# Performance work log

Hardware: AMD Instinct MI355X
Metric: run time of the kernel (lower is better)

The kernel has to match this reference:

```python
import jax, jax.numpy as jnp
import numpy as np

N_NODES = 50000
N_EDGES = 800000
IN_DIM = 128
OUT_DIM = 64
K_KERNELS = 2
S_ATTEN = 2


def setup_inputs() -> dict:
    key = jax.random.key(0)
    ks = jax.random.split(key, 9)
    return {
        "x": jax.random.normal(ks[0], (N_NODES, IN_DIM), dtype=jnp.float32),
        "support_vals": jax.random.uniform(ks[1], (K_KERNELS, N_EDGES), dtype=jnp.float32),
        "atten_vals": jax.random.uniform(ks[2], (S_ATTEN, N_EDGES), dtype=jnp.float32),
        "W_transform": jax.random.normal(ks[3], (K_KERNELS, IN_DIM, OUT_DIM), dtype=jnp.float32) * 0.05,
        "w_left": jax.random.normal(ks[4], (K_KERNELS, S_ATTEN + 1, OUT_DIM), dtype=jnp.float32) * 0.05,
        "w_right": jax.random.normal(ks[5], (K_KERNELS, S_ATTEN + 1, OUT_DIM), dtype=jnp.float32) * 0.05,
        "W_residual": jax.random.normal(ks[6], (IN_DIM + OUT_DIM, OUT_DIM), dtype=jnp.float32) * 0.05,
        "edge_rows": jax.random.randint(ks[7], (N_EDGES,), 0, N_NODES, dtype=jnp.int64),
        "edge_cols": jax.random.randint(ks[8], (N_EDGES,), 0, N_NODES, dtype=jnp.int64),
    }


def reference(x, support_vals, atten_vals, W_transform, w_left, w_right, W_residual, edge_rows, edge_cols):
    # x: [N, F], edge lists: [E]; all supports share the same sparsity pattern.
    N = x.shape[0]
    K = W_transform.shape[0]
    output = jnp.zeros((N, W_transform.shape[2]), dtype=x.dtype)
    for k in range(K):
        wx = x @ W_transform[k]                       # [N, D]
        al = wx @ w_left[k].T                         # [N, S+1]
        ar = wx @ w_right[k].T                        # [N, S+1]
        # per-support edge values; support i=S uses this kernel's Cheb support
        vals = jnp.concatenate([atten_vals, support_vals[k][None, :]], axis=0)  # [S+1, E]
        # score_e = sum_i (al[row_e,i] + ar[col_e,i]) * vals[i,e]
        scores = jnp.einsum('es,se->e', al[edge_rows] + ar[edge_cols], vals)    # [E]
        # row-wise (segment) softmax over nonzeros, as tf.sparse_softmax
        m = jax.ops.segment_max(scores, edge_rows, num_segments=N)              # [N]
        ex = jnp.exp(scores - m[edge_rows])
        denom = jax.ops.segment_sum(ex, edge_rows, num_segments=N)              # [N]
        probs = ex / denom[edge_rows]                                           # [E]
        # spmm: out[r] = sum_{e: row_e=r} probs_e * wx[col_e]
        output = output + jax.ops.segment_sum(probs[:, None] * wx[edge_cols], edge_rows, num_segments=N)
    # residual projection then elu activation
    output = jnp.concatenate([x, output], axis=-1) @ W_residual
    return jax.nn.elu(output)
```

## Files before the change

kernel.cpp:

```cpp
#include <hip/hip_runtime.h>

#define N_NODES 50000
#define N_EDGES 800000
#define IN_DIM 128
#define OUT_DIM 64
#define NEG_INF (-1e30f)
#define GBLK ((N_NODES + 63) / 64)
#define BSHIFT 7
#define NBUK ((N_NODES + 127) >> 7)
#define NBUKP 392
#define EB 1024
#define PREB ((N_EDGES + EB - 1) / EB)
#define NFRAG (3 * 16 + 8)
#define STAGE_CAP 3072

typedef unsigned short ushort_t;
typedef __attribute__((ext_vector_type(8))) short short8;
typedef __attribute__((ext_vector_type(4))) float f32x4;
typedef __attribute__((ext_vector_type(2))) _Float16 half2_t;

__device__ __forceinline__ unsigned f2bf(float f) {
    unsigned u = __float_as_uint(f);
    u += 0x7fffu + ((u >> 16) & 1u);
    return u >> 16;
}
__device__ __forceinline__ unsigned rl_u(unsigned v, int i) {
    return __builtin_amdgcn_readlane(v, i);
}
__device__ __forceinline__ unsigned pack_h2(float a, float b) {
    auto h = __builtin_amdgcn_cvt_pkrtz(a, b);
    union { decltype(h) h2; unsigned u; } v; v.h2 = h; return v.u;
}
__device__ __forceinline__ float dot2u(unsigned w, unsigned p, float acc) {
    union { unsigned u; half2_t h; } wv, pv;
    wv.u = w; pv.u = p;
    return __builtin_amdgcn_fdot2(wv.h, pv.h, acc, false);
}

__global__ void wpack_kernel(const float* __restrict__ Wt,
                             const float* __restrict__ Wres,
                             ushort_t* __restrict__ Wpack) {
    int idx = blockIdx.x * 256 + threadIdx.x;
    if (idx >= NFRAG * 512) return;
    int f = idx >> 9;
    int within = idx & 511;
    int lane = within >> 3;
    int b = within & 7;
    float val;
    if (f < 48) {
        int mat = f >> 4;
        int ct = (f >> 2) & 3;
        int kc = f & 3;
        int k = kc * 32 + (lane >> 4) * 8 + b;
        int c = ct * 16 + (lane & 15);
        const float* W = (mat < 2) ? (Wt + (size_t)mat * IN_DIM * OUT_DIM) : Wres;
        val = W[(size_t)k * OUT_DIM + c];
    } else {
        int f2 = f - 48;
        int ct = f2 >> 1;
        int kc = f2 & 1;
        int k = kc * 32 + (lane >> 4) * 8 + b;
        int c = ct * 16 + (lane & 15);
        val = Wres[(size_t)(IN_DIM + k) * OUT_DIM + c];
    }
    Wpack[idx] = (ushort_t)f2bf(val);
}

__global__ __launch_bounds__(256) void gemm_kernel(
        const float* __restrict__ x,
        const ushort_t* __restrict__ Wpack,
        const float* __restrict__ wl,
        const float* __restrict__ wr,
        unsigned* __restrict__ wxi,
        float* __restrict__ xres,
        float* __restrict__ al,
        float* __restrict__ ar) {
    int wave = threadIdx.x >> 6;
    int lane = threadIdx.x & 63;
    int lr = lane & 15;
    int lg = lane >> 4;
    int row0 = blockIdx.x * 64 + wave * 16;

    int arow = row0 + lr;
    if (arow >= N_NODES) arow = N_NODES - 1;
    const float* xr = x + (size_t)arow * IN_DIM;
    short8 afrag[4];
#pragma unroll
    for (int kc = 0; kc < 4; ++kc) {
        float4 f0 = *(const float4*)(xr + kc * 32 + lg * 8);
        float4 f1 = *(const float4*)(xr + kc * 32 + lg * 8 + 4);
        short8 a;
        a[0] = (short)f2bf(f0.x); a[1] = (short)f2bf(f0.y);
        a[2] = (short)f2bf(f0.z); a[3] = (short)f2bf(f0.w);
        a[4] = (short)f2bf(f1.x); a[5] = (short)f2bf(f1.y);
        a[6] = (short)f2bf(f1.z); a[7] = (short)f2bf(f1.w);
        afrag[kc] = a;
    }

    f32x4 acc[3][4] = {};
#pragma unroll
    for (int kc = 0; kc < 4; ++kc) {
#pragma unroll
        for (int mat = 0; mat < 3; ++mat) {
#pragma unroll
            for (int ct = 0; ct < 4; ++ct) {
                short8 bfrag = *(const short8*)(
                    Wpack + (size_t)(((mat * 4 + ct) * 4 + kc) << 9) + lane * 8);
                acc[mat][ct] = __builtin_amdgcn_mfma_f32_16x16x32_bf16(
                    afrag[kc], bfrag, acc[mat][ct], 0, 0, 0);
            }
        }
    }

#pragma unroll
    for (int r = 0; r < 4; ++r) {
        int gr = row0 + lg * 4 + r;
        if (gr < N_NODES) {
#pragma unroll
            for (int ct = 0; ct < 4; ++ct) {
                wxi[(size_t)gr * OUT_DIM + ct * 16 + lr] =
                    pack_h2(acc[0][ct][r], acc[1][ct][r]);
                xres[(size_t)gr * OUT_DIM + ct * 16 + lr] = acc[2][ct][r];
            }
        }
    }

#pragma unroll
    for (int mat = 0; mat < 2; ++mat) {
#pragma unroll
        for (int s = 0; s < 3; ++s) {
            float wlv[4], wrv[4];
#pragma unroll
            for (int ct = 0; ct < 4; ++ct) {
                wlv[ct] = wl[(size_t)(mat * 3 + s) * OUT_DIM + ct * 16 + lr];
                wrv[ct] = wr[(size_t)(mat * 3 + s) * OUT_DIM + ct * 16 + lr];
            }
#pragma unroll
            for (int r = 0; r < 4; ++r) {
                float pl = 0.f, pr = 0.f;
#pragma unroll
                for (int ct = 0; ct < 4; ++ct) {
                    pl = fmaf(acc[mat][ct][r], wlv[ct], pl);
                    pr = fmaf(acc[mat][ct][r], wrv[ct], pr);
                }
#pragma unroll
                for (int off = 1; off < 16; off <<= 1) {
                    pl += __shfl_xor(pl, off);
                    pr += __shfl_xor(pr, off);
                }
                if (lr == 0) {
                    int gr = row0 + lg * 4 + r;
                    if (gr < N_NODES) {
                        al[(size_t)gr * 6 + mat * 3 + s] = pl;
                        ar[(size_t)gr * 6 + mat * 3 + s] = pr;
                    }
                }
            }
        }
    }
}

__global__ __launch_bounds__(256) void score_sort_kernel(
        const int* __restrict__ rows,
        const int* __restrict__ cols,
        const float* __restrict__ atten,
        const float* __restrict__ support,
        const float* __restrict__ al,
        const float* __restrict__ ar,
        uint4* __restrict__ etmp,
        uint2* __restrict__ cl) {
    __shared__ int cnt[512];
    __shared__ int cur[512];
    __shared__ int aux[256];
    __shared__ uint4 stage[EB];
    int t = threadIdx.x;
    cnt[t] = 0; cnt[t + 256] = 0;
    __syncthreads();
    int base0 = blockIdx.x * EB;
    int nval = min(EB, N_EDGES - base0);

    int r_[4], c_[4];
    float s0_[4], s1_[4];
#pragma unroll
    for (int i = 0; i < 4; ++i) {
        int e = base0 + i * 256 + t;
        bool v = e < N_EDGES;
        int r = v ? rows[e] : -1;
        int c = v ? cols[e] : 0;
        float sc0 = 0.f, sc1 = 0.f;
        if (v) {
            float a0 = atten[e], a1 = atten[N_EDGES + e];
            float sp0 = support[e], sp1 = support[N_EDGES + e];
            const float* A = al + (size_t)r * 6;
            const float* B = ar + (size_t)c * 6;
            sc0 = (A[0] + B[0]) * a0 + (A[1] + B[1]) * a1 + (A[2] + B[2]) * sp0;
            sc1 = (A[3] + B[3]) * a0 + (A[4] + B[4]) * a1 + (A[5] + B[5]) * sp1;
            atomicAdd(&cnt[r >> BSHIFT], 1);
        }
        r_[i] = r; c_[i] = c; s0_[i] = sc0; s1_[i] = sc1;
    }
    __syncthreads();
    int a0 = cnt[2 * t], a1 = cnt[2 * t + 1];
    int ps = a0 + a1;
    aux[t] = ps;
    __syncthreads();
    int val = ps;
    for (int off = 1; off < 256; off <<= 1) {
        int y = (t >= off) ? aux[t - off] : 0;
        __syncthreads();
        val += y; aux[t] = val;
        __syncthreads();
    }
    int e2 = val - ps;
    cur[2 * t] = e2;
    cur[2 * t + 1] = e2 + a0;
    size_t cb = (size_t)blockIdx.x * NBUKP;
    if (2 * t < NBUK)     cl[cb + 2 * t]     = make_uint2((unsigned)a0, (unsigned)e2);
    if (2 * t + 1 < NBUK) cl[cb + 2 * t + 1] = make_uint2((unsigned)a1, (unsigned)(e2 + a0));
    __syncthreads();
#pragma unroll
    for (int i = 0; i < 4; ++i) {
        if (r_[i] < 0) continue;
        int pos = atomicAdd(&cur[r_[i] >> BSHIFT], 1);
        uint4 pv;
        pv.x = (unsigned)c_[i] | ((unsigned)(r_[i] & 127) << 16);
        pv.y = __float_as_uint(s0_[i]);
        pv.z = __float_as_uint(s1_[i]);
        pv.w = 0u;
        stage[pos] = pv;
    }
    __syncthreads();
    for (int i = t; i < nval; i += 256)
        etmp[(size_t)base0 + i] = stage[i];
}

__global__ void colscan_kernel(const uint2* __restrict__ cl,
                               int* __restrict__ btot) {
    __shared__ int sh[256];
    int k = blockIdx.x, t = threadIdx.x;
    int s = 0;
    for (int b = t; b < PREB; b += 256) s += (int)cl[(size_t)b * NBUKP + k].x;
    sh[t] = s;
    __syncthreads();
    for (int off = 128; off > 0; off >>= 1) {
        if (t < off) sh[t] += sh[t + off];
        __syncthreads();
    }
    if (t == 0) btot[k] = sh[0];
}

__global__ __launch_bounds__(256) void sortb_kernel(
        const uint2* __restrict__ cl,
        const int* __restrict__ btot,
        const uint4* __restrict__ etmp,
        uint4* __restrict__ edata,
        int* __restrict__ row_ptr) {
    __shared__ uint4 stage[STAGE_CAP];
    __shared__ int rpos[PREB + 2];
    __shared__ int lloff[PREB];
    __shared__ int aux[256];
    __shared__ int bb[512];
    __shared__ int hist[128], rcur[128];
    int k = blockIdx.x, t = threadIdx.x;

    bb[t] = (t < NBUK) ? btot[t] : 0;
    bb[t + 256] = (t + 256 < NBUK) ? btot[t + 256] : 0;
    __syncthreads();
    int a0 = bb[2 * t], a1 = bb[2 * t + 1];
    int ps = a0 + a1;
    aux[t] = ps;
    __syncthreads();
    int val = ps;
    for (int off = 1; off < 256; off <<= 1) {
        int y = (t >= off) ? aux[t - off] : 0;
        __syncthreads();
        val += y; aux[t] = val;
        __syncthreads();
    }
    bb[2 * t] = val - ps;
    bb[2 * t + 1] = val - ps + a0;
    __syncthreads();
    int base = bb[k];

    for (int b = t; b < PREB; b += 256) {
        uint2 v2 = cl[(size_t)b * NBUKP + k];
        rpos[b] = (int)v2.x;
        lloff[b] = (int)v2.y;
    }
    if (t < 128) hist[t] = 0;
    __syncthreads();
    int v[4];
    int idx4 = 4 * t;
#pragma unroll
    for (int i = 0; i < 4; ++i) v[i] = (idx4 + i < PREB) ? rpos[idx4 + i] : 0;
    __syncthreads();
    int s = 0;
#pragma unroll
    for (int i = 0; i < 4; ++i) { int tmp = v[i]; v[i] = s; s += tmp; }
    aux[t] = s;
    __syncthreads();
    int tv = s;
    for (int off = 1; off < 256; off <<= 1) {
        int y = (t >= off) ? aux[t - off] : 0;
        __syncthreads();
        tv += y; aux[t] = tv;
        __syncthreads();
    }
    int ofs = tv - s;
#pragma unroll
    for (int i = 0; i < 4; ++i)
        if (idx4 + i <= PREB) rpos[idx4 + i] = ofs + v[i];
    __syncthreads();
    int nb = rpos[PREB];

    for (int b = t; b < PREB; b += 256) {
        int s0 = rpos[b];
        int n = rpos[b + 1] - s0;
        int lo = lloff[b];
        const uint4* src = etmp + (size_t)b * EB + lo;
        for (int i = 0; i < n; ++i) {
            uint4 rec = src[i];
            int j = s0 + i;
            if (j < STAGE_CAP) stage[j] = rec;
            atomicAdd(&hist[(rec.x >> 16) & 127], 1);
        }
    }
    __syncthreads();
    int hv = (t < 128) ? hist[t] : 0;
    aux[t] = hv;
    __syncthreads();
    int hval = hv;
    for (int off = 1; off < 128; off <<= 1) {
        int y = (t >= off && t < 128) ? aux[t - off] : 0;
        __syncthreads();
        hval += y; aux[t] = hval;
        __syncthreads();
    }
    if (t < 128) {
        rcur[t] = hval - hv;
        int row = (k << BSHIFT) + t;
        if (row < N_NODES) row_ptr[row] = base + hval - hv;
    }
    if (k == NBUK - 1 && t == 0) row_ptr[N_NODES] = N_EDGES;
    __syncthreads();
    for (int j = t; j < nb; j += 256) {
        uint4 rec;
        if (j < STAGE_CAP) rec = stage[j];
        else {
            int lo = 0, hi = PREB - 1;
            while (lo < hi) { int mid = (lo + hi + 1) >> 1; if (rpos[mid] <= j) lo = mid; else hi = mid - 1; }
            rec = etmp[(size_t)lo * EB + lloff[lo] + (j - rpos[lo])];
        }
        int rl = (rec.x >> 16) & 127;
        int dst = atomicAdd(&rcur[rl], 1);
        edata[(size_t)base + dst] = rec;
    }
}

__global__ void attn_kernel(const int* __restrict__ row_ptr,
                            const uint4* __restrict__ edata,
                            const unsigned* __restrict__ wxi,
                            ushort_t* __restrict__ aacc) {
    int wid = blockIdx.x * 4 + (threadIdx.x >> 6);
    if (wid >= N_NODES) return;
    int lane = threadIdx.x & 63;
    int beg = row_ptr[wid], end = row_ptr[wid + 1];
    int deg = end - beg;
    float a = 0.f;

    if (deg > 0 && deg <= 64) {
        bool valid = lane < deg;
        uint4 ed = edata[valid ? beg + lane : beg];
        unsigned c = ed.x & 0xFFFFu;
        float sc0 = valid ? __uint_as_float(ed.y) : NEG_INF;
        float sc1 = valid ? __uint_as_float(ed.z) : NEG_INF;
        float m0 = sc0, m1 = sc1;
#pragma unroll
        for (int off = 32; off > 0; off >>= 1) {
            m0 = fmaxf(m0, __shfl_xor(m0, off));
            m1 = fmaxf(m1, __shfl_xor(m1, off));
        }
        float e0 = valid ? __expf(sc0 - m0) : 0.f;
        float e1 = valid ? __expf(sc1 - m1) : 0.f;
        float l0 = e0, l1 = e1;
#pragma unroll
        for (int off = 32; off > 0; off >>= 1) {
            l0 += __shfl_xor(l0, off);
            l1 += __shfl_xor(l1, off);
        }
        unsigned pp = pack_h2(e0 / l0, e1 / l1);
        float acc8[8] = {};
        int i = 0;
        for (; i + 8 <= deg; i += 8) {
            unsigned cc[8], vv[8];
#pragma unroll
            for (int j = 0; j < 8; ++j) cc[j] = rl_u(c, i + j);
#pragma unroll
            for (int j = 0; j < 8; ++j) vv[j] = wxi[(size_t)cc[j] * OUT_DIM + lane];
#pragma unroll
            for (int j = 0; j < 8; ++j)
                acc8[j] = dot2u(vv[j], rl_u(pp, i + j), acc8[j]);
        }
        for (; i < deg; ++i) {
            unsigned ci = rl_u(c, i);
            unsigned v = wxi[(size_t)ci * OUT_DIM + lane];
            acc8[0] = dot2u(v, rl_u(pp, i), acc8[0]);
        }
        a = ((acc8[0] + acc8[1]) + (acc8[2] + acc8[3]))
          + ((acc8[4] + acc8[5]) + (acc8[6] + acc8[7]));
    } else if (deg > 64) {
        float m0 = NEG_INF, l0 = 0.f, m1 = NEG_INF, l1 = 0.f;
        for (int base = beg; base < end; base += 64) {
            int pos = base + lane;
            bool valid = pos < end;
            uint4 ed = edata[valid ? pos : beg];
            float sc0 = valid ? __uint_as_float(ed.y) : NEG_INF;
            float sc1 = valid ? __uint_as_float(ed.z) : NEG_INF;
            float cm0 = sc0, cm1 = sc1;
#pragma unroll
            for (int off = 32; off > 0; off >>= 1) {
                cm0 = fmaxf(cm0, __shfl_xor(cm0, off));
                cm1 = fmaxf(cm1, __shfl_xor(cm1, off));
            }
            float mn0 = fmaxf(m0, cm0), mn1 = fmaxf(m1, cm1);
            float e0 = valid ? __expf(sc0 - mn0) : 0.f;
            float e1 = valid ? __expf(sc1 - mn1) : 0.f;
#pragma unroll
            for (int off = 32; off > 0; off >>= 1) {
                e0 += __shfl_xor(e0, off);
                e1 += __shfl_xor(e1, off);
            }
            l0 = l0 * __expf(m0 - mn0) + e0;
            l1 = l1 * __expf(m1 - mn1) + e1;
            m0 = mn0; m1 = mn1;
        }
        float inv0 = 1.f / l0, inv1 = 1.f / l1;
        for (int base = beg; base < end; base += 64) {
            int pos = base + lane;
            bool valid = pos < end;
            uint4 ed = edata[valid ? pos : beg];
            unsigned c = ed.x & 0xFFFFu;
            float p0 = valid ? __expf(__uint_as_float(ed.y) - m0) * inv0 : 0.f;
            float p1 = valid ? __expf(__uint_as_float(ed.z) - m1) * inv1 : 0.f;
            unsigned pp = pack_h2(p0, p1);
            int cnt = min(64, end - base);
            for (int i = 0; i < cnt; ++i) {
                unsigned ci = rl_u(c, i);
                unsigned v = wxi[(size_t)ci * OUT_DIM + lane];
                a = dot2u(v, rl_u(pp, i), a);
            }
        }
    }
    aacc[(size_t)wid * OUT_DIM + lane] = (ushort_t)f2bf(a);
}

__global__ __launch_bounds__(256) void resid_kernel(
        const ushort_t* __restrict__ aacc,
        const float* __restrict__ xres,
        const ushort_t* __restrict__ Wpack,
        float* __restrict__ out) {
    int wave = threadIdx.x >> 6;
    int lane = threadIdx.x & 63;
    int lr = lane & 15;
    int lg = lane >> 4;
    int row0 = blockIdx.x * 64 + wave * 16;
    int arow = row0 + lr;
    if (arow >= N_NODES) arow = N_NODES - 1;
    const ushort_t* ap = aacc + (size_t)arow * OUT_DIM;
    short8 af[2];
#pragma unroll
    for (int kc = 0; kc < 2; ++kc)
        af[kc] = *(const short8*)(ap + kc * 32 + lg * 8);
    f32x4 acc4[4] = {};
#pragma unroll
    for (int kc = 0; kc < 2; ++kc) {
#pragma unroll
        for (int ct = 0; ct < 4; ++ct) {
            short8 bfrag = *(const short8*)(
                Wpack + (size_t)((48 + ct * 2 + kc) << 9) + lane * 8);
            acc4[ct] = __builtin_amdgcn_mfma_f32_16x16x32_bf16(
                af[kc], bfrag, acc4[ct], 0, 0, 0);
        }
    }
#pragma unroll
    for (int r = 0; r < 4; ++r) {
        int gr = row0 + lg * 4 + r;
        if (gr < N_NODES) {
#pragma unroll
            for (int ct = 0; ct < 4; ++ct) {
                float v = acc4[ct][r] + xres[(size_t)gr * OUT_DIM + ct * 16 + lr];
                out[(size_t)gr * OUT_DIM + ct * 16 + lr] = (v > 0.f) ? v : expm1f(v);
            }
        }
    }
}

extern "C" void kernel_launch(void* const* d_in, const int* in_sizes, int n_in,
                              void* d_out, int out_size, void* d_ws, size_t ws_size,
                              hipStream_t stream) {
    const float* x       = (const float*)d_in[0];
    const float* support = (const float*)d_in[1];
    const float* atten   = (const float*)d_in[2];
    const float* Wt      = (const float*)d_in[3];
    const float* wl      = (const float*)d_in[4];
    const float* wr      = (const float*)d_in[5];
    const float* Wres    = (const float*)d_in[6];
    const int*   rows    = (const int*)d_in[7];
    const int*   cols    = (const int*)d_in[8];
    float* out = (float*)d_out;

    unsigned* wxi   = (unsigned*)d_ws;
    float* xres     = (float*)(wxi + (size_t)N_NODES * OUT_DIM);
    float* al       = xres + (size_t)N_NODES * OUT_DIM;
    float* ar       = al + (size_t)N_NODES * 6;
    uint4* etmp     = (uint4*)(ar + (size_t)N_NODES * 6);
    uint4* edata    = etmp + (size_t)N_EDGES;
    int*   row_ptr  = (int*)(edata + (size_t)N_EDGES);
    uint2* cl       = (uint2*)(row_ptr + N_NODES + 4);
    int*   btot     = (int*)(cl + (size_t)PREB * NBUKP);
    ushort_t* Wpack = (ushort_t*)(btot + NBUK + 4);
    ushort_t* aacc  = (ushort_t*)etmp;

    wpack_kernel<<<(NFRAG * 512 + 255) / 256, 256, 0, stream>>>(Wt, Wres, Wpack);
    gemm_kernel<<<GBLK, 256, 0, stream>>>(x, Wpack, wl, wr, wxi, xres, al, ar);
    score_sort_kernel<<<PREB, 256, 0, stream>>>(
        rows, cols, atten, support, al, ar, etmp, cl);
    colscan_kernel<<<NBUK, 256, 0, stream>>>(cl, btot);
    sortb_kernel<<<NBUK, 256, 0, stream>>>(
        cl, btot, etmp, edata, row_ptr);
    attn_kernel<<<(N_NODES + 3) / 4, 256, 0, stream>>>(
        row_ptr, edata, wxi, aacc);
    resid_kernel<<<GBLK, 256, 0, stream>>>(aacc, xres, Wpack, out);
}
```

Baseline: 139.0 us.

## Use fixed-capacity 64-row buckets and drop the bucket-total scan kernel

```diff
diff --git a/kernel.cpp b/kernel.cpp
--- a/kernel.cpp
+++ b/kernel.cpp
@@ -6,13 +6,14 @@
 #define OUT_DIM 64
 #define NEG_INF (-1e30f)
 #define GBLK ((N_NODES + 63) / 64)
-#define BSHIFT 7
-#define NBUK ((N_NODES + 127) >> 7)
-#define NBUKP 392
+#define BSHIFT 6
+#define NBUK ((N_NODES + 63) >> 6)
+#define NBUKP 784
 #define EB 1024
 #define PREB ((N_EDGES + EB - 1) / EB)
 #define NFRAG (3 * 16 + 8)
-#define STAGE_CAP 3072
+#define STAGE_CAP 2048
+#define BUKCAP 2048
 
 typedef unsigned short ushort_t;
 typedef __attribute__((ext_vector_type(8))) short short8;
@@ -169,12 +170,12 @@
         const float* __restrict__ ar,
         uint4* __restrict__ etmp,
         uint2* __restrict__ cl) {
-    __shared__ int cnt[512];
-    __shared__ int cur[512];
+    __shared__ int cnt[1024];
+    __shared__ int cur[1024];
     __shared__ int aux[256];
     __shared__ uint4 stage[EB];
     int t = threadIdx.x;
-    cnt[t] = 0; cnt[t + 256] = 0;
+    cnt[t] = 0; cnt[t + 256] = 0; cnt[t + 512] = 0; cnt[t + 768] = 0;
     __syncthreads();
     int base0 = blockIdx.x * EB;
     int nval = min(EB, N_EDGES - base0);
@@ -200,8 +201,8 @@
         r_[i] = r; c_[i] = c; s0_[i] = sc0; s1_[i] = sc1;
     }
     __syncthreads();
-    int a0 = cnt[2 * t], a1 = cnt[2 * t + 1];
-    int ps = a0 + a1;
+    int v0 = cnt[4 * t], v1 = cnt[4 * t + 1], v2 = cnt[4 * t + 2], v3 = cnt[4 * t + 3];
+    int ps = v0 + v1 + v2 + v3;
     aux[t] = ps;
     __syncthreads();
     int val = ps;
@@ -211,19 +212,25 @@
         val += y; aux[t] = val;
         __syncthreads();
     }
-    int e2 = val - ps;
-    cur[2 * t] = e2;
-    cur[2 * t + 1] = e2 + a0;
+    int e0x = val - ps;
+    cur[4 * t]     = e0x;
+    cur[4 * t + 1] = e0x + v0;
+    cur[4 * t + 2] = e0x + v0 + v1;
+    cur[4 * t + 3] = e0x + v0 + v1 + v2;
     size_t cb = (size_t)blockIdx.x * NBUKP;
-    if (2 * t < NBUK)     cl[cb + 2 * t]     = make_uint2((unsigned)a0, (unsigned)e2);
-    if (2 * t + 1 < NBUK) cl[cb + 2 * t + 1] = make_uint2((unsigned)a1, (unsigned)(e2 + a0));
+    int vv[4] = {v0, v1, v2, v3};
+#pragma unroll
+    for (int j = 0; j < 4; ++j) {
+        int idx = 4 * t + j;
+        if (idx < NBUK) cl[cb + idx] = make_uint2((unsigned)vv[j], (unsigned)cur[idx]);
+    }
     __syncthreads();
 #pragma unroll
     for (int i = 0; i < 4; ++i) {
         if (r_[i] < 0) continue;
         int pos = atomicAdd(&cur[r_[i] >> BSHIFT], 1);
         uint4 pv;
-        pv.x = (unsigned)c_[i] | ((unsigned)(r_[i] & 127) << 16);
+        pv.x = (unsigned)c_[i] | ((unsigned)(r_[i] & 63) << 16);
         pv.y = __float_as_uint(s0_[i]);
         pv.z = __float_as_uint(s1_[i]);
         pv.w = 0u;
@@ -234,60 +241,25 @@
         etmp[(size_t)base0 + i] = stage[i];
 }
 
-__global__ void colscan_kernel(const uint2* __restrict__ cl,
-                               int* __restrict__ btot) {
-    __shared__ int sh[256];
-    int k = blockIdx.x, t = threadIdx.x;
-    int s = 0;
-    for (int b = t; b < PREB; b += 256) s += (int)cl[(size_t)b * NBUKP + k].x;
-    sh[t] = s;
-    __syncthreads();
-    for (int off = 128; off > 0; off >>= 1) {
-        if (t < off) sh[t] += sh[t + off];
-        __syncthreads();
-    }
-    if (t == 0) btot[k] = sh[0];
-}
-
 __global__ __launch_bounds__(256) void sortb_kernel(
         const uint2* __restrict__ cl,
-        const int* __restrict__ btot,
         const uint4* __restrict__ etmp,
         uint4* __restrict__ edata,
-        int* __restrict__ row_ptr) {
+        uint2* __restrict__ rowinfo) {
     __shared__ uint4 stage[STAGE_CAP];
     __shared__ int rpos[PREB + 2];
     __shared__ int lloff[PREB];
     __shared__ int aux[256];
-    __shared__ int bb[512];
-    __shared__ int hist[128], rcur[128];
+    __shared__ int hist[64], rcur[64];
     int k = blockIdx.x, t = threadIdx.x;
-
-    bb[t] = (t < NBUK) ? btot[t] : 0;
-    bb[t + 256] = (t + 256 < NBUK) ? btot[t + 256] : 0;
-    __syncthreads();
-    int a0 = bb[2 * t], a1 = bb[2 * t + 1];
-    int ps = a0 + a1;
-    aux[t] = ps;
-    __syncthreads();
-    int val = ps;
-    for (int off = 1; off < 256; off <<= 1) {
-        int y = (t >= off) ? aux[t - off] : 0;
-        __syncthreads();
-        val += y; aux[t] = val;
-        __syncthreads();
-    }
-    bb[2 * t] = val - ps;
-    bb[2 * t + 1] = val - ps + a0;
-    __syncthreads();
-    int base = bb[k];
+    int base = k * BUKCAP;
 
     for (int b = t; b < PREB; b += 256) {
         uint2 v2 = cl[(size_t)b * NBUKP + k];
         rpos[b] = (int)v2.x;
         lloff[b] = (int)v2.y;
     }
-    if (t < 128) hist[t] = 0;
+    if (t < 64) hist[t] = 0;
     __syncthreads();
     int v[4];
     int idx4 = 4 * t;
@@ -322,26 +294,27 @@
             uint4 rec = src[i];
             int j = s0 + i;
             if (j < STAGE_CAP) stage[j] = rec;
-            atomicAdd(&hist[(rec.x >> 16) & 127], 1);
-        }
-    }
-    __syncthreads();
-    int hv = (t < 128) ? hist[t] : 0;
+            atomicAdd(&hist[(rec.x >> 16) & 63], 1);
+        }
+    }
+    __syncthreads();
+    int hv = (t < 64) ? hist[t] : 0;
     aux[t] = hv;
     __syncthreads();
     int hval = hv;
-    for (int off = 1; off < 128; off <<= 1) {
-        int y = (t >= off && t < 128) ? aux[t - off] : 0;
+    for (int off = 1; off < 64; off <<= 1) {
+        int y = (t >= off && t < 64) ? aux[t - off] : 0;
         __syncthreads();
         hval += y; aux[t] = hval;
         __syncthreads();
     }
-    if (t < 128) {
-        rcur[t] = hval - hv;
+    if (t < 64) {
+        int start = hval - hv;
+        rcur[t] = start;
         int row = (k << BSHIFT) + t;
-        if (row < N_NODES) row_ptr[row] = base + hval - hv;
-    }
-    if (k == NBUK - 1 && t == 0) row_ptr[N_NODES] = N_EDGES;
+        if (row < N_NODES)
+            rowinfo[row] = make_uint2((unsigned)(base + start), (unsigned)hv);
+    }
     __syncthreads();
     for (int j = t; j < nb; j += 256) {
         uint4 rec;
@@ -351,21 +324,22 @@
             while (lo < hi) { int mid = (lo + hi + 1) >> 1; if (rpos[mid] <= j) lo = mid; else hi = mid - 1; }
             rec = etmp[(size_t)lo * EB + lloff[lo] + (j - rpos[lo])];
         }
-        int rl = (rec.x >> 16) & 127;
+        int rl = (rec.x >> 16) & 63;
         int dst = atomicAdd(&rcur[rl], 1);
-        edata[(size_t)base + dst] = rec;
-    }
-}
-
-__global__ void attn_kernel(const int* __restrict__ row_ptr,
+        if (dst < BUKCAP) edata[(size_t)base + dst] = rec;
+    }
+}
+
+__global__ void attn_kernel(const uint2* __restrict__ rowinfo,
                             const uint4* __restrict__ edata,
                             const unsigned* __restrict__ wxi,
                             ushort_t* __restrict__ aacc) {
     int wid = blockIdx.x * 4 + (threadIdx.x >> 6);
     if (wid >= N_NODES) return;
     int lane = threadIdx.x & 63;
-    int beg = row_ptr[wid], end = row_ptr[wid + 1];
-    int deg = end - beg;
+    uint2 ri = rowinfo[wid];
+    int beg = (int)ri.x;
+    int deg = (int)ri.y;
     float a = 0.f;
 
     if (deg > 0 && deg <= 64) {
@@ -409,6 +383,7 @@
         a = ((acc8[0] + acc8[1]) + (acc8[2] + acc8[3]))
           + ((acc8[4] + acc8[5]) + (acc8[6] + acc8[7]));
     } else if (deg > 64) {
+        int end = beg + deg;
         float m0 = NEG_INF, l0 = 0.f, m1 = NEG_INF, l1 = 0.f;
         for (int base = beg; base < end; base += 64) {
             int pos = base + lane;
@@ -515,20 +490,17 @@
     float* ar       = al + (size_t)N_NODES * 6;
     uint4* etmp     = (uint4*)(ar + (size_t)N_NODES * 6);
     uint4* edata    = etmp + (size_t)N_EDGES;
-    int*   row_ptr  = (int*)(edata + (size_t)N_EDGES);
-    uint2* cl       = (uint2*)(row_ptr + N_NODES + 4);
-    int*   btot     = (int*)(cl + (size_t)PREB * NBUKP);
-    ushort_t* Wpack = (ushort_t*)(btot + NBUK + 4);
+    uint2* rowinfo  = (uint2*)(edata + (size_t)NBUK * BUKCAP);
+    uint2* cl       = rowinfo + N_NODES + 4;
+    ushort_t* Wpack = (ushort_t*)(cl + (size_t)PREB * NBUKP);
     ushort_t* aacc  = (ushort_t*)etmp;
 
     wpack_kernel<<<(NFRAG * 512 + 255) / 256, 256, 0, stream>>>(Wt, Wres, Wpack);
     gemm_kernel<<<GBLK, 256, 0, stream>>>(x, Wpack, wl, wr, wxi, xres, al, ar);
     score_sort_kernel<<<PREB, 256, 0, stream>>>(
         rows, cols, atten, support, al, ar, etmp, cl);
-    colscan_kernel<<<NBUK, 256, 0, stream>>>(cl, btot);
-    sortb_kernel<<<NBUK, 256, 0, stream>>>(
-        cl, btot, etmp, edata, row_ptr);
+    sortb_kernel<<<NBUK, 256, 0, stream>>>(cl, etmp, edata, rowinfo);
     attn_kernel<<<(N_NODES + 3) / 4, 256, 0, stream>>>(
-        row_ptr, edata, wxi, aacc);
+        rowinfo, edata, wxi, aacc);
     resid_kernel<<<GBLK, 256, 0, stream>>>(aacc, xres, Wpack, out);
 }
```

Result: faster. 129.9 us (-6.5%).
